# Performance work log

Measured on AMD Instinct MI355X. Metric: run time of the kernel, lower is better.

Reference implementation:

```python
import jax, jax.numpy as jnp
import numpy as np

N = 100000   # nodes
E = 1600000  # edges (avg degree 16)
HID = 128    # in_feats = n_hidden
P = 100000   # pos/neg link pairs
L = 3        # GIN layers
BN_EPS = 1e-5


def setup_inputs() -> dict:
    key = jax.random.key(0)
    ks = jax.random.split(key, 16)
    s = 1.0 / np.sqrt(HID)  # ~ torch linear init scale
    inp = {
        "x": jax.random.normal(ks[0], (N, HID), jnp.float32),
        "src": jax.random.randint(ks[1], (E,), 0, N, jnp.int32),
        "dst": jax.random.randint(ks[2], (E,), 0, N, jnp.int32),
        "pos_src": jax.random.randint(ks[3], (P,), 0, N, jnp.int32),
        "pos_dst": jax.random.randint(ks[4], (P,), 0, N, jnp.int32),
        "neg_src": jax.random.randint(ks[5], (P,), 0, N, jnp.int32),
        "neg_dst": jax.random.randint(ks[6], (P,), 0, N, jnp.int32),
        "W0": jax.random.normal(ks[7], (L, HID, HID), jnp.float32) * s,
        "W1": jax.random.normal(ks[8], (L, HID, HID), jnp.float32) * s,
        "g_mlp": jnp.ones((L, HID), jnp.float32),
        "b_mlp": jnp.zeros((L, HID), jnp.float32),
        "g_apply": jnp.ones((L, HID), jnp.float32),
        "b_apply": jnp.zeros((L, HID), jnp.float32),
        "g_out": jnp.ones((L - 1, HID), jnp.float32),
        "b_out": jnp.zeros((L - 1, HID), jnp.float32),
        "pW1": jax.random.normal(ks[9], (HID, HID), jnp.float32) * s,
        "pb1": jnp.zeros((HID,), jnp.float32),
        "pW2": jax.random.normal(ks[10], (HID, HID), jnp.float32) * s,
        "pb2": jnp.zeros((HID,), jnp.float32),
        "pW3": jax.random.normal(ks[11], (1, HID), jnp.float32) * s,
        "pb3": jnp.zeros((1,), jnp.float32),
    }
    return inp


def _bn(h, g, b):
    # training-mode BatchNorm1d: batch stats, biased variance
    mu = jnp.mean(h, axis=0)
    var = jnp.mean(jnp.square(h - mu), axis=0)
    return g * (h - mu) * jax.lax.rsqrt(var + BN_EPS) + b


def reference(x, src, dst, pos_src, pos_dst, neg_src, neg_dst,
              W0, W1, g_mlp, b_mlp, g_apply, b_apply, g_out, b_out,
              pW1, pb1, pW2, pb2, pW3, pb3):
    # in-degree for mean aggregation (clamped to avoid div-by-zero)
    deg = jnp.maximum(
        jax.ops.segment_sum(jnp.ones((E,), x.dtype), dst, num_segments=N), 1.0)
    h = x
    for l in range(L):
        # GINConv, eps = 0: h_dst + mean over in-neighbors
        agg = jax.ops.segment_sum(h[src], dst, num_segments=N) / deg[:, None]
        z = h + agg
        # ApplyNodeFunc: MLP(2 layers, no bias) with inner BN+ReLU, then BN+ReLU
        m = jax.nn.relu(_bn(z @ W0[l].T, g_mlp[l], b_mlp[l]))
        m = m @ W1[l].T
        h = jax.nn.relu(_bn(m, g_apply[l], b_apply[l]))
        if l < L - 1:
            # outer BN + ReLU (dropout is identity in eval)
            h = jax.nn.relu(_bn(h, g_out[l], b_out[l]))

    def predict(hs, hd):
        t = hs * hd
        t = jax.nn.relu(t @ pW1.T + pb1)
        t = jax.nn.relu(t @ pW2.T + pb2)
        return t @ pW3.T + pb3  # [P, 1]

    h_pos = predict(h[pos_src], h[pos_dst])
    h_neg = predict(h[neg_src], h[neg_dst])
    return (h_pos, h_neg)
```

## Files before the change

kernel.cpp:

```cpp
#include <hip/hip_runtime.h>

#define HID 128
#define BN_EPS 1e-5f
#define PSHIFT 9
#define PBW 512

typedef __bf16 bf16;
typedef __attribute__((ext_vector_type(8))) __bf16 bf16x8;
typedef __attribute__((ext_vector_type(2))) __bf16 bf16x2;
typedef __attribute__((ext_vector_type(4))) float f32x4;

__device__ __forceinline__ float bnrelu(float x, float a, float c) {
  return fmaxf(fmaf(a, x, c), 0.f);
}

__global__ void hist_k(const int* __restrict__ dst, int* __restrict__ cnt, int E) {
  int i = blockIdx.x * blockDim.x + threadIdx.x;
  if (i < E) atomicAdd(&cnt[dst[i]], 1);
}

__global__ __launch_bounds__(256)
void scan1_k(const int* __restrict__ cnt, int* __restrict__ bsum, int Nn) {
  __shared__ int red[4];
  int tid = threadIdx.x;
  int base = blockIdx.x * 1024;
  int s = 0;
#pragma unroll
  for (int u = 0; u < 4; ++u) {
    int i = base + u * 256 + tid;
    if (i < Nn) s += cnt[i];
  }
#pragma unroll
  for (int d = 1; d < 64; d <<= 1) s += __shfl_xor(s, d, 64);
  int lane = tid & 63, wv = tid >> 6;
  if (lane == 0) red[wv] = s;
  __syncthreads();
  if (tid == 0) bsum[blockIdx.x] = red[0] + red[1] + red[2] + red[3];
}

__global__ void scan2_k(int* __restrict__ bsum, int G) {
  int lane = threadIdx.x;
  int carry = 0;
  for (int base = 0; base < G; base += 64) {
    int i = base + lane;
    int v = (i < G) ? bsum[i] : 0;
    int x = v;
#pragma unroll
    for (int d = 1; d < 64; d <<= 1) { int t = __shfl_up(x, d, 64); if (lane >= d) x += t; }
    if (i < G) bsum[i] = carry + x - v;
    carry += __shfl(x, 63, 64);
  }
}

__global__ __launch_bounds__(256)
void scan3_k(const int* __restrict__ cnt, const int* __restrict__ boff,
             int* __restrict__ row_start, int Nn, int E) {
  __shared__ int wtot[4];
  int tid = threadIdx.x, lane = tid & 63, wv = tid >> 6;
  int i0 = blockIdx.x * 1024 + tid * 4;
  int t0 = 0, t1 = 0, t2 = 0, t3 = 0;
  if (i0 + 3 < Nn) {
    int4 v = *(const int4*)(cnt + i0);
    t0 = v.x; t1 = v.y; t2 = v.z; t3 = v.w;
  } else {
    if (i0     < Nn) t0 = cnt[i0];
    if (i0 + 1 < Nn) t1 = cnt[i0 + 1];
    if (i0 + 2 < Nn) t2 = cnt[i0 + 2];
    if (i0 + 3 < Nn) t3 = cnt[i0 + 3];
  }
  int tsum = t0 + t1 + t2 + t3;
  int x = tsum;
#pragma unroll
  for (int d = 1; d < 64; d <<= 1) { int t = __shfl_up(x, d, 64); if (lane >= d) x += t; }
  if (lane == 63) wtot[wv] = x;
  __syncthreads();
  int wo = 0;
  for (int k = 0; k < wv; ++k) wo += wtot[k];
  int base = boff[blockIdx.x] + wo + x - tsum;
  if (i0     < Nn) row_start[i0] = base;
  if (i0 + 1 < Nn) row_start[i0 + 1] = base + t0;
  if (i0 + 2 < Nn) row_start[i0 + 2] = base + t0 + t1;
  if (i0 + 3 < Nn) row_start[i0 + 3] = base + t0 + t1 + t2;
  if (blockIdx.x == 0 && tid == 0) row_start[Nn] = E;
}

__global__ void initb_k(const int* __restrict__ row_start, int* __restrict__ bcur,
                        int Nn, int NB2) {
  int i = threadIdx.x;
  if (i < NB2) {
    int n = i << PSHIFT; if (n > Nn) n = Nn;
    bcur[i] = row_start[n];
  }
}

__global__ __launch_bounds__(256)
void partb_k(const int* __restrict__ src, const int* __restrict__ dst,
             int* __restrict__ bcur, unsigned* __restrict__ ebuf2, int E, int NB2) {
  __shared__ int lcnt[256], gbase[256], lcur[256];
  int tid = threadIdx.x;
  if (tid < NB2 || tid < 256) { lcnt[tid] = 0; lcur[tid] = 0; }
  __syncthreads();
  int base = blockIdx.x * 2048;
  int ok[8]; unsigned pk[8]; int bk[8];
#pragma unroll
  for (int u = 0; u < 8; ++u) {
    int e = base + u * 256 + tid;
    if (e < E) {
      int s = src[e], d = dst[e];
      ok[u] = 1; bk[u] = d >> PSHIFT;
      pk[u] = ((unsigned)(d & (PBW - 1)) << 17) | (unsigned)s;
      atomicAdd(&lcnt[bk[u]], 1);
    } else ok[u] = 0;
  }
  __syncthreads();
  if (tid < NB2 && lcnt[tid]) gbase[tid] = atomicAdd(&bcur[tid], lcnt[tid]);
  __syncthreads();
#pragma unroll
  for (int u = 0; u < 8; ++u) if (ok[u]) {
    int sl = atomicAdd(&lcur[bk[u]], 1);
    ebuf2[gbase[bk[u]] + sl] = pk[u];
  }
}

__global__ __launch_bounds__(512)
void fillb_k(const unsigned* __restrict__ ebuf2, const int* __restrict__ row_start,
             int* __restrict__ csr, int Nn) {
  __shared__ int ncur[PBW];
  int tid = threadIdx.x;
  if (tid < PBW) ncur[tid] = 0;
  __syncthreads();
  int nb0 = blockIdx.x << PSHIFT;
  int hi = nb0 + PBW; if (hi > Nn) hi = Nn;
  int beg = row_start[nb0], end = row_start[hi];
  for (int e = beg + tid; e < end; e += 512) {
    unsigned v = ebuf2[e];
    int dl = v >> 17, s = (int)(v & 0x1FFFF);
    int p = atomicAdd(&ncur[dl], 1);
    csr[row_start[nb0 + dl] + p] = s;
  }
}

__global__ __launch_bounds__(256)
void wconv_k(const float* __restrict__ W0, const float* __restrict__ W1,
             const float* __restrict__ pW1, const float* __restrict__ pW2,
             bf16* __restrict__ Wb) {
  int idx = (blockIdx.x * 256 + threadIdx.x) * 4;
  int seg = idx >> 14, loc = idx & 16383;
  const float* srcp = seg < 3 ? W0 + (size_t)seg * 16384
                    : seg < 6 ? W1 + (size_t)(seg - 3) * 16384
                    : seg == 6 ? pW1 : pW2;
  float4 v = *(const float4*)(srcp + loc);
  union { bf16 h[4]; unsigned long long u; } pk;
  pk.h[0] = (bf16)v.x; pk.h[1] = (bf16)v.y; pk.h[2] = (bf16)v.z; pk.h[3] = (bf16)v.w;
  *(unsigned long long*)(Wb + idx) = pk.u;
}

__global__ __launch_bounds__(256)
void xconv_k(const float* __restrict__ X, bf16* __restrict__ Xh, int total) {
  int idx = (blockIdx.x * 256 + threadIdx.x) * 4;
  if (idx >= total) return;
  float4 v = *(const float4*)(X + idx);
  union { bf16 h[4]; unsigned long long u; } pk;
  pk.h[0] = (bf16)v.x; pk.h[1] = (bf16)v.y; pk.h[2] = (bf16)v.z; pk.h[3] = (bf16)v.w;
  *(unsigned long long*)(Xh + idx) = pk.u;
}

template<int MODE>
__global__ __launch_bounds__(256)
void agg_k(const bf16* __restrict__ Hh,
           const float* __restrict__ ac, const float* __restrict__ g, const float* __restrict__ b,
           float invN,
           const int* __restrict__ row_start, const int* __restrict__ csr,
           bf16* __restrict__ Z, int Nn) {
  __shared__ float sA[128], sC[128];
  int tid = threadIdx.x;
  if (MODE) {
    if (tid < 128) {
      float mu = ac[tid] * invN;
      float var = fmaxf(ac[128 + tid] * invN - mu * mu, 0.f);
      float a = g[tid] * rsqrtf(var + BN_EPS);
      sA[tid] = a; sC[tid] = fmaf(-a, mu, b[tid]);
    }
    __syncthreads();
  }
  int wv = tid >> 6, lane = tid & 63;
  int n = blockIdx.x * 4 + wv;
  if (n >= Nn) return;
  int c0 = lane * 2;
  float Ax = 0, Ay = 0, Cx = 0, Cy = 0;
  if (MODE) { Ax = sA[c0]; Ay = sA[c0 + 1]; Cx = sC[c0]; Cy = sC[c0 + 1]; }
  int beg = row_start[n], end = row_start[n + 1];
  bf16x2 hn = *(const bf16x2*)(Hh + (size_t)n * HID + c0);
  float inv = 1.f / fmaxf((float)(end - beg), 1.f);
  float ax0 = 0, ay0 = 0, ax1 = 0, ay1 = 0, ax2 = 0, ay2 = 0, ax3 = 0, ay3 = 0;
  int j = beg;
  for (; j + 8 <= end; j += 8) {
    int s0 = csr[j], s1 = csr[j + 1], s2 = csr[j + 2], s3 = csr[j + 3];
    int s4 = csr[j + 4], s5 = csr[j + 5], s6 = csr[j + 6], s7 = csr[j + 7];
    bf16x2 v0 = *(const bf16x2*)(Hh + (size_t)s0 * HID + c0);
    bf16x2 v1 = *(const bf16x2*)(Hh + (size_t)s1 * HID + c0);
    bf16x2 v2 = *(const bf16x2*)(Hh + (size_t)s2 * HID + c0);
    bf16x2 v3 = *(const bf16x2*)(Hh + (size_t)s3 * HID + c0);
    bf16x2 v4 = *(const bf16x2*)(Hh + (size_t)s4 * HID + c0);
    bf16x2 v5 = *(const bf16x2*)(Hh + (size_t)s5 * HID + c0);
    bf16x2 v6 = *(const bf16x2*)(Hh + (size_t)s6 * HID + c0);
    bf16x2 v7 = *(const bf16x2*)(Hh + (size_t)s7 * HID + c0);
    float x0 = (float)v0[0], y0 = (float)v0[1], x1 = (float)v1[0], y1 = (float)v1[1];
    float x2 = (float)v2[0], y2 = (float)v2[1], x3 = (float)v3[0], y3 = (float)v3[1];
    float x4 = (float)v4[0], y4 = (float)v4[1], x5 = (float)v5[0], y5 = (float)v5[1];
    float x6 = (float)v6[0], y6 = (float)v6[1], x7 = (float)v7[0], y7 = (float)v7[1];
    if (MODE) {
      x0 = bnrelu(x0, Ax, Cx); y0 = bnrelu(y0, Ay, Cy);
      x1 = bnrelu(x1, Ax, Cx); y1 = bnrelu(y1, Ay, Cy);
      x2 = bnrelu(x2, Ax, Cx); y2 = bnrelu(y2, Ay, Cy);
      x3 = bnrelu(x3, Ax, Cx); y3 = bnrelu(y3, Ay, Cy);
      x4 = bnrelu(x4, Ax, Cx); y4 = bnrelu(y4, Ay, Cy);
      x5 = bnrelu(x5, Ax, Cx); y5 = bnrelu(y5, Ay, Cy);
      x6 = bnrelu(x6, Ax, Cx); y6 = bnrelu(y6, Ay, Cy);
      x7 = bnrelu(x7, Ax, Cx); y7 = bnrelu(y7, Ay, Cy);
    }
    ax0 += x0; ay0 += y0; ax1 += x1; ay1 += y1;
    ax2 += x2; ay2 += y2; ax3 += x3; ay3 += y3;
    ax0 += x4; ay0 += y4; ax1 += x5; ay1 += y5;
    ax2 += x6; ay2 += y6; ax3 += x7; ay3 += y7;
  }
  for (; j < end; ++j) {
    int s = csr[j];
    bf16x2 v = *(const bf16x2*)(Hh + (size_t)s * HID + c0);
    float vx = (float)v[0], vy = (float)v[1];
    if (MODE) { vx = bnrelu(vx, Ax, Cx); vy = bnrelu(vy, Ay, Cy); }
    ax0 += vx; ay0 += vy;
  }
  float ax = (ax0 + ax1) + (ax2 + ax3);
  float ay = (ay0 + ay1) + (ay2 + ay3);
  float hx = (float)hn[0], hy = (float)hn[1];
  if (MODE) { hx = bnrelu(hx, Ax, Cx); hy = bnrelu(hy, Ay, Cy); }
  float zx = hx + ax * inv, zy = hy + ay * inv;
  union { bf16 h[2]; unsigned u; } pk;
  pk.h[0] = (bf16)zx; pk.h[1] = (bf16)zy;
  *(unsigned*)((char*)Z + ((size_t)n * HID + c0) * 2) = pk.u;
}

template<int AMODE, int OUTF>
__global__ __launch_bounds__(256)
void gemm_k(const bf16* __restrict__ Asrc,
            const float* __restrict__ acIn, const float* __restrict__ g, const float* __restrict__ b,
            float invN,
            const bf16* __restrict__ Wb, bf16* __restrict__ Cb, float* __restrict__ Cf,
            float* __restrict__ accumOut, int Nrows) {
  __shared__ float sA[128], sC[128], sSum[128], sSq[128];
  int tid = threadIdx.x;
  if (tid < 128) {
    sSum[tid] = 0.f; sSq[tid] = 0.f;
    if (AMODE) {
      float mu = acIn[tid] * invN;
      float var = fmaxf(acIn[128 + tid] * invN - mu * mu, 0.f);
      float a = g[tid] * rsqrtf(var + BN_EPS);
      sA[tid] = a; sC[tid] = fmaf(-a, mu, b[tid]);
    }
  }
  __syncthreads();
  int wv = tid >> 6, lane = tid & 63;
  int lm = lane & 15, lg = lane >> 4;
  int rowbase = blockIdx.x * 128 + wv * 32;
  f32x4 acc[2][8] = {};
#pragma unroll
  for (int kk = 0; kk < 4; ++kk) {
    int kb = kk * 32 + lg * 8;
    bf16x8 af[2];
#pragma unroll
    for (int rt = 0; rt < 2; ++rt) {
      int row = rowbase + rt * 16 + lm; if (row > Nrows - 1) row = Nrows - 1;
      bf16x8 raw = *(const bf16x8*)(Asrc + (size_t)row * HID + kb);
      if (AMODE == 0) {
        af[rt] = raw;
      } else {
        float4 a0 = *(const float4*)(sA + kb), a1 = *(const float4*)(sA + kb + 4);
        float4 q0 = *(const float4*)(sC + kb), q1 = *(const float4*)(sC + kb + 4);
        bf16x8 f;
        f[0] = (bf16)bnrelu((float)raw[0], a0.x, q0.x); f[1] = (bf16)bnrelu((float)raw[1], a0.y, q0.y);
        f[2] = (bf16)bnrelu((float)raw[2], a0.z, q0.z); f[3] = (bf16)bnrelu((float)raw[3], a0.w, q0.w);
        f[4] = (bf16)bnrelu((float)raw[4], a1.x, q1.x); f[5] = (bf16)bnrelu((float)raw[5], a1.y, q1.y);
        f[6] = (bf16)bnrelu((float)raw[6], a1.z, q1.z); f[7] = (bf16)bnrelu((float)raw[7], a1.w, q1.w);
        af[rt] = f;
      }
    }
    bf16x8 bfr[8];
#pragma unroll
    for (int ct = 0; ct < 8; ++ct)
      bfr[ct] = *(const bf16x8*)(Wb + (size_t)(ct * 16 + lm) * HID + kb);
#pragma unroll
    for (int rt = 0; rt < 2; ++rt)
#pragma unroll
      for (int ct = 0; ct < 8; ++ct)
        acc[rt][ct] = __builtin_amdgcn_mfma_f32_16x16x32_bf16(af[rt], bfr[ct], acc[rt][ct], 0, 0, 0);
  }
#pragma unroll
  for (int ct = 0; ct < 8; ++ct) {
    int col = ct * 16 + lm;
    float ps = 0.f, pq = 0.f;
#pragma unroll
    for (int rt = 0; rt < 2; ++rt) {
#pragma unroll
      for (int i = 0; i < 4; ++i) {
        int row = rowbase + rt * 16 + lg * 4 + i;
        if (row < Nrows) {
          float v = acc[rt][ct][i];
          if (OUTF) Cf[(size_t)row * HID + col] = v;
          else      Cb[(size_t)row * HID + col] = (bf16)v;
          ps += v; pq = fmaf(v, v, pq);
        }
      }
    }
    ps += __shfl_xor(ps, 16, 64); ps += __shfl_xor(ps, 32, 64);
    pq += __shfl_xor(pq, 16, 64); pq += __shfl_xor(pq, 32, 64);
    if (lane < 16) { atomicAdd(&sSum[col], ps); atomicAdd(&sSq[col], pq); }
  }
  __syncthreads();
  if (tid < 128) {
    atomicAdd(&accumOut[tid], sSum[tid]);
    atomicAdd(&accumOut[128 + tid], sSq[tid]);
  }
}

__global__ __launch_bounds__(256)
void stats1_k(const float* __restrict__ T, const float* __restrict__ acIn,
              const float* __restrict__ g, const float* __restrict__ b, float invN,
              float* __restrict__ accumOut, bf16* __restrict__ Y, int Nrows) {
  int col = threadIdx.x & 127, half = threadIdx.x >> 7;
  float mu = acIn[col] * invN;
  float var = fmaxf(acIn[128 + col] * invN - mu * mu, 0.f);
  float av = g[col] * rsqrtf(var + BN_EPS);
  float cv = fmaf(-av, mu, b[col]);
  float s = 0.f, sq = 0.f;
  for (int r = blockIdx.x * 2 + half; r < Nrows; r += gridDim.x * 2) {
    float x = T[(size_t)r * HID + col];
    x = fmaxf(fmaf(av, x, cv), 0.f);
    Y[(size_t)r * HID + col] = (bf16)x;
    s += x; sq = fmaf(x, x, sq);
  }
  __shared__ float sb[256], qb[256];
  sb[threadIdx.x] = s; qb[threadIdx.x] = sq;
  __syncthreads();
  if (half == 0) {
    s += sb[threadIdx.x + 128]; sq += qb[threadIdx.x + 128];
    atomicAdd(&accumOut[col], s); atomicAdd(&accumOut[128 + col], sq);
  }
}

__global__ __launch_bounds__(512)
void pred_k(const float* __restrict__ T, const float* __restrict__ acIn,
            const float* __restrict__ g, const float* __restrict__ b, float invN,
            const int* __restrict__ ps, const int* __restrict__ pd,
            const int* __restrict__ ns, const int* __restrict__ nd,
            const bf16* __restrict__ W1b, const float* __restrict__ b1p,
            const bf16* __restrict__ W2b, const float* __restrict__ b2p,
            const float* __restrict__ w3, const float* __restrict__ b3,
            float* __restrict__ out, int Pn) {
  __shared__ bf16 At[128 * 128];
  __shared__ float sAp[128], sCp[128];
  int tid = threadIdx.x;
  if (tid < 128) {
    float mu = acIn[tid] * invN;
    float var = fmaxf(acIn[128 + tid] * invN - mu * mu, 0.f);
    float a = g[tid] * rsqrtf(var + BN_EPS);
    sAp[tid] = a; sCp[tid] = fmaf(-a, mu, b[tid]);
  }
  __syncthreads();
  int q0 = blockIdx.x * 128;
  {
    int r = tid >> 2;
    int q = q0 + r;
    int cb = (tid & 3) * 32;
    if (q < 2 * Pn) {
      int s, d;
      if (q < Pn) { s = ps[q]; d = pd[q]; } else { s = ns[q - Pn]; d = nd[q - Pn]; }
      const float* rs_ = T + (size_t)s * HID;
      const float* rd_ = T + (size_t)d * HID;
#pragma unroll
      for (int c = cb; c < cb + 32; c += 4) {
        float4 xs = *(const float4*)(rs_ + c);
        float4 xd = *(const float4*)(rd_ + c);
        float4 av = *(const float4*)(sAp + c);
        float4 cv = *(const float4*)(sCp + c);
        float t0 = bnrelu(xs.x, av.x, cv.x) * bnrelu(xd.x, av.x, cv.x);
        float t1 = bnrelu(xs.y, av.y, cv.y) * bnrelu(xd.y, av.y, cv.y);
        float t2 = bnrelu(xs.z, av.z, cv.z) * bnrelu(xd.z, av.z, cv.z);
        float t3 = bnrelu(xs.w, av.w, cv.w) * bnrelu(xd.w, av.w, cv.w);
        union { bf16 h[4]; unsigned long long u; } pk;
        pk.h[0] = (bf16)t0; pk.h[1] = (bf16)t1; pk.h[2] = (bf16)t2; pk.h[3] = (bf16)t3;
        unsigned addr = (unsigned)(r * 256 + c * 2);
        addr ^= (unsigned)((r & 7) << 4);
        *(unsigned long long*)((char*)At + addr) = pk.u;
      }
    } else {
#pragma unroll
      for (int c = cb; c < cb + 32; c += 4) {
        unsigned addr = (unsigned)(r * 256 + c * 2);
        addr ^= (unsigned)((r & 7) << 4);
        *(unsigned long long*)((char*)At + addr) = 0ull;
      }
    }
  }
  __syncthreads();
  int wv = tid >> 6, lane = tid & 63;
  int lm = lane & 15, lg = lane >> 4;
  const f32x4 vzero = {0.f, 0.f, 0.f, 0.f};
  f32x4 acc[8];
#pragma unroll
  for (int c = 0; c < 8; ++c) acc[c] = vzero;
  int rowA = wv * 16 + lm;
#pragma unroll
  for (int kk = 0; kk < 4; ++kk) {
    unsigned addr = (unsigned)(rowA * 256 + kk * 64 + lg * 16);
    addr ^= (unsigned)((rowA & 7) << 4);
    bf16x8 af = *(const bf16x8*)((char*)At + addr);
    bf16x8 bfr[8];
#pragma unroll
    for (int ct = 0; ct < 8; ++ct)
      bfr[ct] = *(const bf16x8*)(W1b + (size_t)(ct * 16 + lm) * HID + kk * 32 + lg * 8);
#pragma unroll
    for (int ct = 0; ct < 8; ++ct)
      acc[ct] = __builtin_amdgcn_mfma_f32_16x16x32_bf16(af, bfr[ct], acc[ct], 0, 0, 0);
  }
  __syncthreads();
#pragma unroll
  for (int ct = 0; ct < 8; ++ct) {
    int col = ct * 16 + lm;
    float bb = b1p[col];
#pragma unroll
    for (int i = 0; i < 4; ++i) {
      int row = wv * 16 + lg * 4 + i;
      float v = fmaxf(acc[ct][i] + bb, 0.f);
      unsigned addr = (unsigned)(row * 256 + col * 2);
      addr ^= (unsigned)((row & 7) << 4);
      *(bf16*)((char*)At + addr) = (bf16)v;
    }
  }
  __syncthreads();
#pragma unroll
  for (int c = 0; c < 8; ++c) acc[c] = vzero;
#pragma unroll
  for (int kk = 0; kk < 4; ++kk) {
    unsigned addr = (unsigned)(rowA * 256 + kk * 64 + lg * 16);
    addr ^= (unsigned)((rowA & 7) << 4);
    bf16x8 af = *(const bf16x8*)((char*)At + addr);
    bf16x8 bfr[8];
#pragma unroll
    for (int ct = 0; ct < 8; ++ct)
      bfr[ct] = *(const bf16x8*)(W2b + (size_t)(ct * 16 + lm) * HID + kk * 32 + lg * 8);
#pragma unroll
    for (int ct = 0; ct < 8; ++ct)
      acc[ct] = __builtin_amdgcn_mfma_f32_16x16x32_bf16(af, bfr[ct], acc[ct], 0, 0, 0);
  }
  float b2v[8], w3v[8];
#pragma unroll
  for (int ct = 0; ct < 8; ++ct) { b2v[ct] = b2p[ct * 16 + lm]; w3v[ct] = w3[ct * 16 + lm]; }
  float b3s = b3[0];
#pragma unroll
  for (int i = 0; i < 4; ++i) {
    float p = 0.f;
#pragma unroll
    for (int ct = 0; ct < 8; ++ct)
      p += fmaxf(acc[ct][i] + b2v[ct], 0.f) * w3v[ct];
    p += __shfl_xor(p, 1); p += __shfl_xor(p, 2);
    p += __shfl_xor(p, 4); p += __shfl_xor(p, 8);
    int row = wv * 16 + lg * 4 + i;
    int q = q0 + row;
    if (lm == 0 && q < 2 * Pn) out[q] = p + b3s;
  }
}

extern "C" void kernel_launch(void* const* d_in, const int* in_sizes, int n_in,
                              void* d_out, int out_size, void* d_ws, size_t ws_size,
                              hipStream_t stream) {
  const float* x  = (const float*)d_in[0];
  const int* src  = (const int*)d_in[1];
  const int* dst  = (const int*)d_in[2];
  const int* ps   = (const int*)d_in[3];
  const int* pd   = (const int*)d_in[4];
  const int* ns   = (const int*)d_in[5];
  const int* nd   = (const int*)d_in[6];
  const float* W0 = (const float*)d_in[7];
  const float* W1 = (const float*)d_in[8];
  const float* g_mlp   = (const float*)d_in[9];
  const float* b_mlp   = (const float*)d_in[10];
  const float* g_apply = (const float*)d_in[11];
  const float* b_apply = (const float*)d_in[12];
  const float* g_out   = (const float*)d_in[13];
  const float* b_out   = (const float*)d_in[14];
  const float* pW1 = (const float*)d_in[15];
  const float* pb1 = (const float*)d_in[16];
  const float* pW2 = (const float*)d_in[17];
  const float* pb2 = (const float*)d_in[18];
  const float* pW3 = (const float*)d_in[19];
  const float* pb3 = (const float*)d_in[20];
  float* out = (float*)d_out;

  const int N = in_sizes[0] / HID;
  const int E = in_sizes[1];
  const int P = in_sizes[3];
  const int NB2 = (N + PBW - 1) >> PSHIFT;

  char* w = (char*)d_ws;
  size_t off = 0;
  auto alloc = [&](size_t bytes) -> void* {
    void* p = w + off;
    off = (off + bytes + 255) & ~(size_t)255;
    return p;
  };
  bf16*  Z   = (bf16*)alloc((size_t)N * HID * 2);
  bf16*  TAb = (bf16*)alloc((size_t)N * HID * 2);
  float* TB  = (float*)alloc((size_t)N * HID * 4);
  bf16*  Yb  = (bf16*)alloc((size_t)N * HID * 2);
  bf16*  Xh  = (bf16*)alloc((size_t)N * HID * 2);
  int*   csr = (int*)alloc((size_t)E * 4);
  unsigned* ebuf2 = (unsigned*)alloc((size_t)E * 4);
  int*   row_start = (int*)alloc((size_t)(N + 1) * 4);
  size_t zoff = off;
  int*   cnt   = (int*)alloc((size_t)N * 4);
  float* accum = (float*)alloc(9 * 256 * 4);
  size_t zbytes = off - zoff;
  int*   bsum   = (int*)alloc(256 * 4);
  int*   bcur   = (int*)alloc(256 * 4);
  bf16*  Wb = (bf16*)alloc(8 * 16384 * 2);
  (void)ws_size; (void)n_in; (void)out_size;

  const int G = (N + 1023) / 1024;
  const float invN = 1.f / (float)N;

  hipMemsetAsync(w + zoff, 0, zbytes, stream);
  int gridE = (E + 255) / 256;
  hist_k<<<gridE, 256, 0, stream>>>(dst, cnt, E);
  scan1_k<<<G, 256, 0, stream>>>(cnt, bsum, N);
  scan2_k<<<1, 64, 0, stream>>>(bsum, G);
  scan3_k<<<G, 256, 0, stream>>>(cnt, bsum, row_start, N, E);
  initb_k<<<1, 256, 0, stream>>>(row_start, bcur, N, NB2);
  partb_k<<<(E + 2047) / 2048, 256, 0, stream>>>(src, dst, bcur, ebuf2, E, NB2);
  fillb_k<<<NB2, 512, 0, stream>>>(ebuf2, row_start, csr, N);
  wconv_k<<<128, 256, 0, stream>>>(W0, W1, pW1, pW2, Wb);
  xconv_k<<<(N * HID / 4 + 255) / 256, 256, 0, stream>>>(x, Xh, N * HID);

  int gridN4 = (N + 3) / 4;
  int gridG  = (N + 127) / 128;

  for (int l = 0; l < 3; ++l) {
    int s0 = l * 3 + 0, s1 = l * 3 + 1, s2 = l * 3 + 2;
    if (l == 0)
      agg_k<0><<<gridN4, 256, 0, stream>>>(Xh, nullptr, nullptr, nullptr, invN,
                                           row_start, csr, Z, N);
    else {
      int p2 = (l - 1) * 3 + 2;
      agg_k<1><<<gridN4, 256, 0, stream>>>(Yb,
                                           accum + p2 * 256, g_out + (l - 1) * HID, b_out + (l - 1) * HID,
                                           invN, row_start, csr, Z, N);
    }
    gemm_k<0, 0><<<gridG, 256, 0, stream>>>(Z, nullptr, nullptr, nullptr, invN,
                                            Wb + (size_t)l * 16384, TAb, nullptr,
                                            accum + s0 * 256, N);
    gemm_k<1, 1><<<gridG, 256, 0, stream>>>(TAb, accum + s0 * 256, g_mlp + l * HID, b_mlp + l * HID,
                                            invN, Wb + (size_t)(3 + l) * 16384, nullptr, TB,
                                            accum + s1 * 256, N);
    if (l < 2)
      stats1_k<<<512, 256, 0, stream>>>(TB, accum + s1 * 256, g_apply + l * HID, b_apply + l * HID,
                                        invN, accum + s2 * 256, Yb, N);
  }
  int gridP = (2 * P + 127) / 128;
  pred_k<<<gridP, 512, 0, stream>>>(TB, accum + 7 * 256, g_apply + 2 * HID, b_apply + 2 * HID, invN,
                                    ps, pd, ns, nd,
                                    Wb + (size_t)6 * 16384, pb1,
                                    Wb + (size_t)7 * 16384, pb2,
                                    pW3, pb3, out, P);
}
```

Before: 953.9 us.

## Gather predictor inputs directly into MFMA fragments and halve pred_k block size

The predictor kernel no longer stages the BN+ReLU'd hadamard product through shared memory. Each lane now gathers its source and destination rows straight into bf16 MFMA A-fragments. The block shrinks from 512 to 256 threads, and each wave handles two 16-row tiles, so every W1/W2 fragment load is reused across two MFMAs. This removes one LDS round trip and a barrier but doubles accumulator registers per thread. The partb_k shared-memory init condition is also simplified, which has no effect.

```diff
diff --git a/kernel.cpp b/kernel.cpp
--- a/kernel.cpp
+++ b/kernel.cpp
@@ -98,7 +98,7 @@
              int* __restrict__ bcur, unsigned* __restrict__ ebuf2, int E, int NB2) {
   __shared__ int lcnt[256], gbase[256], lcur[256];
   int tid = threadIdx.x;
-  if (tid < NB2 || tid < 256) { lcnt[tid] = 0; lcur[tid] = 0; }
+  lcnt[tid] = 0; lcur[tid] = 0;
   __syncthreads();
   int base = blockIdx.x * 2048;
   int ok[8]; unsigned pk[8]; int bk[8];
@@ -348,7 +348,7 @@
   }
 }
 
-__global__ __launch_bounds__(512)
+__global__ __launch_bounds__(256)
 void pred_k(const float* __restrict__ T, const float* __restrict__ acIn,
             const float* __restrict__ g, const float* __restrict__ b, float invN,
             const int* __restrict__ ps, const int* __restrict__ pd,
@@ -367,107 +367,110 @@
     sAp[tid] = a; sCp[tid] = fmaf(-a, mu, b[tid]);
   }
   __syncthreads();
-  int q0 = blockIdx.x * 128;
-  {
-    int r = tid >> 2;
-    int q = q0 + r;
-    int cb = (tid & 3) * 32;
-    if (q < 2 * Pn) {
-      int s, d;
-      if (q < Pn) { s = ps[q]; d = pd[q]; } else { s = ns[q - Pn]; d = nd[q - Pn]; }
-      const float* rs_ = T + (size_t)s * HID;
-      const float* rd_ = T + (size_t)d * HID;
-#pragma unroll
-      for (int c = cb; c < cb + 32; c += 4) {
-        float4 xs = *(const float4*)(rs_ + c);
-        float4 xd = *(const float4*)(rd_ + c);
-        float4 av = *(const float4*)(sAp + c);
-        float4 cv = *(const float4*)(sCp + c);
-        float t0 = bnrelu(xs.x, av.x, cv.x) * bnrelu(xd.x, av.x, cv.x);
-        float t1 = bnrelu(xs.y, av.y, cv.y) * bnrelu(xd.y, av.y, cv.y);
-        float t2 = bnrelu(xs.z, av.z, cv.z) * bnrelu(xd.z, av.z, cv.z);
-        float t3 = bnrelu(xs.w, av.w, cv.w) * bnrelu(xd.w, av.w, cv.w);
-        union { bf16 h[4]; unsigned long long u; } pk;
-        pk.h[0] = (bf16)t0; pk.h[1] = (bf16)t1; pk.h[2] = (bf16)t2; pk.h[3] = (bf16)t3;
-        unsigned addr = (unsigned)(r * 256 + c * 2);
-        addr ^= (unsigned)((r & 7) << 4);
-        *(unsigned long long*)((char*)At + addr) = pk.u;
-      }
-    } else {
-#pragma unroll
-      for (int c = cb; c < cb + 32; c += 4) {
-        unsigned addr = (unsigned)(r * 256 + c * 2);
-        addr ^= (unsigned)((r & 7) << 4);
-        *(unsigned long long*)((char*)At + addr) = 0ull;
-      }
-    }
-  }
-  __syncthreads();
   int wv = tid >> 6, lane = tid & 63;
   int lm = lane & 15, lg = lane >> 4;
+  int q0 = blockIdx.x * 128;
+  const float* rsp[2]; const float* rdp[2];
+#pragma unroll
+  for (int rt = 0; rt < 2; ++rt) {
+    int q = q0 + wv * 32 + rt * 16 + lm;
+    if (q >= 2 * Pn) q = 2 * Pn - 1;
+    int s, d;
+    if (q < Pn) { s = ps[q]; d = pd[q]; } else { s = ns[q - Pn]; d = nd[q - Pn]; }
+    rsp[rt] = T + (size_t)s * HID;
+    rdp[rt] = T + (size_t)d * HID;
+  }
   const f32x4 vzero = {0.f, 0.f, 0.f, 0.f};
-  f32x4 acc[8];
-#pragma unroll
-  for (int c = 0; c < 8; ++c) acc[c] = vzero;
-  int rowA = wv * 16 + lm;
+  f32x4 acc[2][8];
+#pragma unroll
+  for (int r = 0; r < 2; ++r) for (int c = 0; c < 8; ++c) acc[r][c] = vzero;
 #pragma unroll
   for (int kk = 0; kk < 4; ++kk) {
-    unsigned addr = (unsigned)(rowA * 256 + kk * 64 + lg * 16);
-    addr ^= (unsigned)((rowA & 7) << 4);
-    bf16x8 af = *(const bf16x8*)((char*)At + addr);
+    int kb = kk * 32 + lg * 8;
+    float4 a0 = *(const float4*)(sAp + kb), a1 = *(const float4*)(sAp + kb + 4);
+    float4 c0 = *(const float4*)(sCp + kb), c1 = *(const float4*)(sCp + kb + 4);
+    bf16x8 af[2];
+#pragma unroll
+    for (int rt = 0; rt < 2; ++rt) {
+      float4 xs0 = *(const float4*)(rsp[rt] + kb), xs1 = *(const float4*)(rsp[rt] + kb + 4);
+      float4 xd0 = *(const float4*)(rdp[rt] + kb), xd1 = *(const float4*)(rdp[rt] + kb + 4);
+      bf16x8 f;
+      f[0] = (bf16)(bnrelu(xs0.x, a0.x, c0.x) * bnrelu(xd0.x, a0.x, c0.x));
+      f[1] = (bf16)(bnrelu(xs0.y, a0.y, c0.y) * bnrelu(xd0.y, a0.y, c0.y));
+      f[2] = (bf16)(bnrelu(xs0.z, a0.z, c0.z) * bnrelu(xd0.z, a0.z, c0.z));
+      f[3] = (bf16)(bnrelu(xs0.w, a0.w, c0.w) * bnrelu(xd0.w, a0.w, c0.w));
+      f[4] = (bf16)(bnrelu(xs1.x, a1.x, c1.x) * bnrelu(xd1.x, a1.x, c1.x));
+      f[5] = (bf16)(bnrelu(xs1.y, a1.y, c1.y) * bnrelu(xd1.y, a1.y, c1.y));
+      f[6] = (bf16)(bnrelu(xs1.z, a1.z, c1.z) * bnrelu(xd1.z, a1.z, c1.z));
+      f[7] = (bf16)(bnrelu(xs1.w, a1.w, c1.w) * bnrelu(xd1.w, a1.w, c1.w));
+      af[rt] = f;
+    }
     bf16x8 bfr[8];
 #pragma unroll
     for (int ct = 0; ct < 8; ++ct)
-      bfr[ct] = *(const bf16x8*)(W1b + (size_t)(ct * 16 + lm) * HID + kk * 32 + lg * 8);
-#pragma unroll
-    for (int ct = 0; ct < 8; ++ct)
-      acc[ct] = __builtin_amdgcn_mfma_f32_16x16x32_bf16(af, bfr[ct], acc[ct], 0, 0, 0);
-  }
-  __syncthreads();
-#pragma unroll
-  for (int ct = 0; ct < 8; ++ct) {
-    int col = ct * 16 + lm;
-    float bb = b1p[col];
-#pragma unroll
-    for (int i = 0; i < 4; ++i) {
-      int row = wv * 16 + lg * 4 + i;
-      float v = fmaxf(acc[ct][i] + bb, 0.f);
-      unsigned addr = (unsigned)(row * 256 + col * 2);
+      bfr[ct] = *(const bf16x8*)(W1b + (size_t)(ct * 16 + lm) * HID + kb);
+#pragma unroll
+    for (int rt = 0; rt < 2; ++rt)
+#pragma unroll
+      for (int ct = 0; ct < 8; ++ct)
+        acc[rt][ct] = __builtin_amdgcn_mfma_f32_16x16x32_bf16(af[rt], bfr[ct], acc[rt][ct], 0, 0, 0);
+  }
+#pragma unroll
+  for (int rt = 0; rt < 2; ++rt)
+#pragma unroll
+    for (int ct = 0; ct < 8; ++ct) {
+      int col = ct * 16 + lm;
+      float bb = b1p[col];
+#pragma unroll
+      for (int i = 0; i < 4; ++i) {
+        int row = wv * 32 + rt * 16 + lg * 4 + i;
+        float v = fmaxf(acc[rt][ct][i] + bb, 0.f);
+        unsigned addr = (unsigned)(row * 256 + col * 2);
+        addr ^= (unsigned)((row & 7) << 4);
+        *(bf16*)((char*)At + addr) = (bf16)v;
+      }
+    }
+  __syncthreads();
+#pragma unroll
+  for (int r = 0; r < 2; ++r) for (int c = 0; c < 8; ++c) acc[r][c] = vzero;
+#pragma unroll
+  for (int kk = 0; kk < 4; ++kk) {
+    bf16x8 af[2];
+#pragma unroll
+    for (int rt = 0; rt < 2; ++rt) {
+      int row = wv * 32 + rt * 16 + lm;
+      unsigned addr = (unsigned)(row * 256 + kk * 64 + lg * 16);
       addr ^= (unsigned)((row & 7) << 4);
-      *(bf16*)((char*)At + addr) = (bf16)v;
-    }
-  }
-  __syncthreads();
-#pragma unroll
-  for (int c = 0; c < 8; ++c) acc[c] = vzero;
-#pragma unroll
-  for (int kk = 0; kk < 4; ++kk) {
-    unsigned addr = (unsigned)(rowA * 256 + kk * 64 + lg * 16);
-    addr ^= (unsigned)((rowA & 7) << 4);
-    bf16x8 af = *(const bf16x8*)((char*)At + addr);
+      af[rt] = *(const bf16x8*)((char*)At + addr);
+    }
     bf16x8 bfr[8];
 #pragma unroll
     for (int ct = 0; ct < 8; ++ct)
       bfr[ct] = *(const bf16x8*)(W2b + (size_t)(ct * 16 + lm) * HID + kk * 32 + lg * 8);
 #pragma unroll
-    for (int ct = 0; ct < 8; ++ct)
-      acc[ct] = __builtin_amdgcn_mfma_f32_16x16x32_bf16(af, bfr[ct], acc[ct], 0, 0, 0);
+    for (int rt = 0; rt < 2; ++rt)
+#pragma unroll
+      for (int ct = 0; ct < 8; ++ct)
+        acc[rt][ct] = __builtin_amdgcn_mfma_f32_16x16x32_bf16(af[rt], bfr[ct], acc[rt][ct], 0, 0, 0);
   }
   float b2v[8], w3v[8];
 #pragma unroll
   for (int ct = 0; ct < 8; ++ct) { b2v[ct] = b2p[ct * 16 + lm]; w3v[ct] = w3[ct * 16 + lm]; }
   float b3s = b3[0];
 #pragma unroll
-  for (int i = 0; i < 4; ++i) {
-    float p = 0.f;
-#pragma unroll
-    for (int ct = 0; ct < 8; ++ct)
-      p += fmaxf(acc[ct][i] + b2v[ct], 0.f) * w3v[ct];
-    p += __shfl_xor(p, 1); p += __shfl_xor(p, 2);
-    p += __shfl_xor(p, 4); p += __shfl_xor(p, 8);
-    int row = wv * 16 + lg * 4 + i;
-    int q = q0 + row;
-    if (lm == 0 && q < 2 * Pn) out[q] = p + b3s;
+  for (int rt = 0; rt < 2; ++rt) {
+#pragma unroll
+    for (int i = 0; i < 4; ++i) {
+      float p = 0.f;
+#pragma unroll
+      for (int ct = 0; ct < 8; ++ct)
+        p += fmaxf(acc[rt][ct][i] + b2v[ct], 0.f) * w3v[ct];
+      p += __shfl_xor(p, 1); p += __shfl_xor(p, 2);
+      p += __shfl_xor(p, 4); p += __shfl_xor(p, 8);
+      int row = wv * 32 + rt * 16 + lg * 4 + i;
+      int q = q0 + row;
+      if (lm == 0 && q < 2 * Pn) out[q] = p + b3s;
+    }
   }
 }
 
@@ -566,7 +569,7 @@
                                         invN, accum + s2 * 256, Yb, N);
   }
   int gridP = (2 * P + 127) / 128;
-  pred_k<<<gridP, 512, 0, stream>>>(TB, accum + 7 * 256, g_apply + 2 * HID, b_apply + 2 * HID, invN,
+  pred_k<<<gridP, 256, 0, stream>>>(TB, accum + 7 * 256, g_apply + 2 * HID, b_apply + 2 * HID, invN,
                                     ps, pd, ns, nd,
                                     Wb + (size_t)6 * 16384, pb1,
                                     Wb + (size_t)7 * 16384, pb2,
```

Result: faster. 892.1 us (-6.5%).
